# Kernel tuning notes

Hardware: AMD Instinct MI355X
Metric: run time of the kernel (lower is better)

## Reference

```python
import jax, jax.numpy as jnp
import numpy as np

ECNUM = 100
CA1NUM = 100
CA3NUM = 100
ACTNUM = 2
TRACKLEN = 100
SIGMA = 5.0
BS = 4096


def setup_inputs() -> dict:
    key = jax.random.key(0)
    ks = jax.random.split(key, 10)
    cue_train = jax.random.randint(ks[0], (BS, TRACKLEN), 0, 3).astype(jnp.int32) - 1  # values in {-1,0,1}
    ec3_last = jax.random.uniform(ks[1], (BS, ECNUM), dtype=jnp.float32)
    ec5_last = jax.random.uniform(ks[2], (BS, ECNUM), dtype=jnp.float32)
    ca1_last = jnp.zeros((BS, CA1NUM), dtype=jnp.float32)
    cueL = (jax.random.uniform(ks[3], (ECNUM,)) < 0.2).astype(jnp.float32)
    cueR = (jax.random.uniform(ks[4], (ECNUM,)) < 0.2).astype(jnp.float32)
    Wec3ca1 = 0.01 * jax.random.uniform(ks[5], (ECNUM, CA1NUM), dtype=jnp.float32)
    Wca3ca1 = 0.01 * jax.random.uniform(ks[6], (CA3NUM, CA1NUM), dtype=jnp.float32)
    Wca1ec5 = 0.01 * jax.random.normal(ks[7], (CA1NUM, ECNUM), dtype=jnp.float32)
    Wca1act = 0.01 * jax.random.uniform(ks[8], (CA1NUM, ACTNUM), dtype=jnp.float32)
    ca1bias = 0.01 * jax.random.uniform(ks[9], (CA1NUM,), dtype=jnp.float32)
    return {
        "bs": BS,
        "cue_train": cue_train,
        "ec3_last": ec3_last,
        "ec5_last": ec5_last,
        "ca1_last": ca1_last,
        "cueL": cueL,
        "cueR": cueR,
        "Wec3ca1": Wec3ca1,
        "Wca3ca1": Wca3ca1,
        "Wca1ec5": Wca1ec5,
        "Wca1act": Wca1act,
        "ca1bias": ca1bias,
    }


def reference(bs, cue_train, ec3_last, ec5_last, ca1_last, cueL, cueR,
              Wec3ca1, Wca3ca1, Wca1ec5, Wca1act, ca1bias):
    # Precompute position-dependent CA3 activity for every timestep: [T, ca3num]
    centers = jnp.linspace(0.0, float(TRACKLEN), CA3NUM)
    xs = jnp.arange(TRACKLEN, dtype=jnp.float32)
    ca3_all = jnp.exp(-(((xs[:, None] - centers[None, :]) / SIGMA) ** 2) / 2.0)
    drive = ca3_all @ Wca3ca1  # [T, ca1num]

    # Sensory input per timestep via conditional gather: [T, bs, ecnum]
    cue_t = cue_train.T[:, :, None]  # [T, bs, 1]
    sensory = jnp.where(cue_t == 1, cueL[None, None, :],
                        jnp.where(cue_t == -1, cueR[None, None, :], 0.0))

    def step(carry, inp):
        ec3, ec5 = carry
        d, s = inp  # d: [ca1num], s: [bs, ecnum]
        ca1 = jax.nn.relu(d[None, :] * (1.0 + jax.nn.sigmoid(ec3 @ Wec3ca1)) - ca1bias)
        ec5 = ec5 + ca1 @ Wca1ec5
        ec5 = 0.69 + 0.3 * jax.nn.sigmoid(4.0 * (ec5 - 0.3))
        ec3 = ec5 * ec3 + s
        return (ec3, ec5), ca1

    (ec3, ec5), ca1his = jax.lax.scan(step, (ec3_last, ec5_last), (drive, sensory))
    ca1 = ca1his[-1]
    actCell = ca1 @ Wca1act
    return actCell, ca1his, ec3, ec5, ca1
```

## Files before the change

### kernel.cpp

```cpp
#include <hip/hip_runtime.h>

#define TLEN 100
#define ECN  100
#define CA1N 100
#define CA3N 100
#define BSZ  4096
#define ACTN 2
#define BT   16
#define SPF  132
#define SPB  136

typedef short bf16x8 __attribute__((ext_vector_type(8)));
typedef float f32x4  __attribute__((ext_vector_type(4)));

__device__ __forceinline__ unsigned short f2bf(float f){
  union { float f; unsigned int u; } c; c.f = f;
  unsigned int u = c.u;
  unsigned int r = (u + 0x7FFFu + ((u >> 16) & 1u)) >> 16;
  return (unsigned short)r;
}
__device__ __forceinline__ float sigm(float x){ return 1.0f / (1.0f + __expf(-x)); }

__global__ void drive_kernel(const float* __restrict__ Wca3ca1, float* __restrict__ drive){
  __shared__ float ca3row[CA3N];
  const int t = blockIdx.x, tid = threadIdx.x;
  if (tid < CA3N){
    float c = (float)tid * (100.0f / 99.0f);
    float d = ((float)t - c) * 0.2f;
    ca3row[tid] = __expf(-0.5f * d * d);
  }
  __syncthreads();
  if (tid < CA1N){
    float acc = 0.f;
    for (int k = 0; k < CA3N; ++k) acc = fmaf(ca3row[k], Wca3ca1[k*CA1N + tid], acc);
    drive[t*CA1N + tid] = acc;
  }
}

__global__ __launch_bounds__(512, 1)
void rnn_kernel(const int*   __restrict__ cue_train,
                const float* __restrict__ ec3_last,
                const float* __restrict__ ec5_last,
                const float* __restrict__ cueL,
                const float* __restrict__ cueR,
                const float* __restrict__ Wec3ca1,
                const float* __restrict__ Wca1ec5,
                const float* __restrict__ Wca1act,
                const float* __restrict__ ca1bias,
                const float* __restrict__ drive,
                float*       __restrict__ out)
{
  __shared__ __align__(16) float ec3f[BT * SPF];
  __shared__ __align__(16) float ec5f[BT * SPF];
  __shared__ __align__(16) float ca1f[BT * SPF];
  __shared__ __align__(16) unsigned short ec3b[BT * SPB];
  __shared__ __align__(16) unsigned short ca1b[BT * SPB];
  __shared__ signed char cueT[TLEN * BT];

  const int tid = threadIdx.x;
  const int b0  = blockIdx.x * BT;

  float* out_act = out;
  float* out_his = out + (size_t)BSZ * ACTN;
  float* out_e3  = out_his + (size_t)TLEN * BSZ * CA1N;
  float* out_e5  = out_e3 + (size_t)BSZ * ECN;
  float* out_c1  = out_e5 + (size_t)BSZ * ECN;

  for (int idx = tid; idx < BT * SPB; idx += 512){ ec3b[idx] = 0; ca1b[idx] = 0; }
  __syncthreads();

  for (int idx = tid; idx < BT * ECN; idx += 512){
    int r = idx / ECN, c = idx - r * ECN;
    float v3 = ec3_last[(size_t)(b0 + r) * ECN + c];
    ec3f[r * SPF + c] = v3;
    ec3b[r * SPB + c] = f2bf(v3);
    ec5f[r * SPF + c] = ec5_last[(size_t)(b0 + r) * ECN + c];
  }
  for (int idx = tid; idx < BT * TLEN; idx += 512){
    int t = idx >> 4, r = idx & 15;
    cueT[idx] = (signed char)cue_train[(size_t)(b0 + r) * TLEN + t];
  }

  const int lane  = tid & 63;
  const int wv    = tid >> 6;
  const int col16 = lane & 15;
  const int q     = lane >> 4;
  const int col   = wv * 16 + col16;
  const bool okc  = (col < CA1N);

  bf16x8 b1[4], b2[4];
  #pragma unroll
  for (int ks = 0; ks < 4; ++ks){
    #pragma unroll
    for (int jj = 0; jj < 8; ++jj){
      int k = ks * 32 + q * 8 + jj;
      float w1 = 0.f, w2 = 0.f;
      if (k < ECN && okc){
        w1 = Wec3ca1[k * CA1N + col];
        w2 = Wca1ec5[k * ECN  + col];
      }
      b1[ks][jj] = (short)f2bf(w1);
      b2[ks][jj] = (short)f2bf(w2);
    }
  }
  float bias_c = 0.f, cL = 0.f, cR = 0.f;
  if (okc){ bias_c = ca1bias[col]; cL = cueL[col]; cR = cueR[col]; }
  __syncthreads();

  const int m = col16;
  const unsigned short* arow1 = &ec3b[m * SPB];
  const unsigned short* arow2 = &ca1b[m * SPB];

  for (int t = 0; t < TLEN; ++t){
    float dv = okc ? drive[t * CA1N + col] : 0.f;

    f32x4 accA = {0.f,0.f,0.f,0.f}, accB = {0.f,0.f,0.f,0.f};
    {
      bf16x8 a0 = *reinterpret_cast<const bf16x8*>(arow1 +  0 + q * 8);
      bf16x8 a1 = *reinterpret_cast<const bf16x8*>(arow1 + 32 + q * 8);
      bf16x8 a2 = *reinterpret_cast<const bf16x8*>(arow1 + 64 + q * 8);
      bf16x8 a3 = *reinterpret_cast<const bf16x8*>(arow1 + 96 + q * 8);
      accA = __builtin_amdgcn_mfma_f32_16x16x32_bf16(a0, b1[0], accA, 0, 0, 0);
      accB = __builtin_amdgcn_mfma_f32_16x16x32_bf16(a1, b1[1], accB, 0, 0, 0);
      accA = __builtin_amdgcn_mfma_f32_16x16x32_bf16(a2, b1[2], accA, 0, 0, 0);
      accB = __builtin_amdgcn_mfma_f32_16x16x32_bf16(a3, b1[3], accB, 0, 0, 0);
    }
    f32x4 z = accA + accB;
    #pragma unroll
    for (int i = 0; i < 4; ++i){
      int r = q * 4 + i;
      float c1 = fmaxf(fmaf(dv, 1.0f + sigm(z[i]), -bias_c), 0.f);
      if (okc){
        out_his[(size_t)t * (BSZ * CA1N) + (size_t)(b0 + r) * CA1N + col] = c1;
        ca1b[r * SPB + col] = f2bf(c1);
        if (t == TLEN - 1) ca1f[r * SPF + col] = c1;
      }
    }
    __syncthreads();

    f32x4 acc2A = {0.f,0.f,0.f,0.f}, acc2B = {0.f,0.f,0.f,0.f};
    {
      bf16x8 a0 = *reinterpret_cast<const bf16x8*>(arow2 +  0 + q * 8);
      bf16x8 a1 = *reinterpret_cast<const bf16x8*>(arow2 + 32 + q * 8);
      bf16x8 a2 = *reinterpret_cast<const bf16x8*>(arow2 + 64 + q * 8);
      bf16x8 a3 = *reinterpret_cast<const bf16x8*>(arow2 + 96 + q * 8);
      acc2A = __builtin_amdgcn_mfma_f32_16x16x32_bf16(a0, b2[0], acc2A, 0, 0, 0);
      acc2B = __builtin_amdgcn_mfma_f32_16x16x32_bf16(a1, b2[1], acc2B, 0, 0, 0);
      acc2A = __builtin_amdgcn_mfma_f32_16x16x32_bf16(a2, b2[2], acc2A, 0, 0, 0);
      acc2B = __builtin_amdgcn_mfma_f32_16x16x32_bf16(a3, b2[3], acc2B, 0, 0, 0);
    }
    f32x4 z2 = acc2A + acc2B;
    int cu4 = *reinterpret_cast<const int*>(&cueT[t * BT + q * 4]);
    #pragma unroll
    for (int i = 0; i < 4; ++i){
      int r = q * 4 + i;
      if (okc){
        float x  = ec5f[r * SPF + col] + z2[i];
        float e5 = fmaf(0.3f, sigm(fmaf(4.0f, x, -1.2f)), 0.69f);
        ec5f[r * SPF + col] = e5;
        int cu = (int)(signed char)(cu4 >> (8 * i));
        float sns = (cu == 1) ? cL : ((cu == -1) ? cR : 0.0f);
        float e3 = fmaf(e5, ec3f[r * SPF + col], sns);
        ec3f[r * SPF + col] = e3;
        ec3b[r * SPB + col] = f2bf(e3);
      }
    }
    __syncthreads();
  }

  if (tid < BT * ACTN){
    int r = tid >> 1, a = tid & 1;
    float acc = 0.f;
    for (int jj = 0; jj < CA1N; ++jj)
      acc = fmaf(ca1f[r * SPF + jj], Wca1act[jj * ACTN + a], acc);
    out_act[(size_t)(b0 + r) * ACTN + a] = acc;
  }
  for (int idx = tid; idx < BT * ECN; idx += 512){
    int r = idx / ECN, c = idx - r * ECN;
    size_t g = (size_t)(b0 + r) * ECN + c;
    out_e3[g] = ec3f[r * SPF + c];
    out_e5[g] = ec5f[r * SPF + c];
    out_c1[g] = ca1f[r * SPF + c];
  }
}

extern "C" void kernel_launch(void* const* d_in, const int* in_sizes, int n_in,
                              void* d_out, int out_size, void* d_ws, size_t ws_size,
                              hipStream_t stream) {
  (void)in_sizes; (void)n_in; (void)out_size; (void)ws_size;
  const int*   cue_train = (const int*)  d_in[1];
  const float* ec3_last  = (const float*)d_in[2];
  const float* ec5_last  = (const float*)d_in[3];
  const float* cueL      = (const float*)d_in[5];
  const float* cueR      = (const float*)d_in[6];
  const float* Wec3ca1   = (const float*)d_in[7];
  const float* Wca3ca1   = (const float*)d_in[8];
  const float* Wca1ec5   = (const float*)d_in[9];
  const float* Wca1act   = (const float*)d_in[10];
  const float* ca1bias   = (const float*)d_in[11];
  float* out   = (float*)d_out;
  float* drive = (float*)d_ws;

  drive_kernel<<<TLEN, 128, 0, stream>>>(Wca3ca1, drive);
  rnn_kernel<<<BSZ / BT, 512, 0, stream>>>(cue_train, ec3_last, ec5_last,
                                           cueL, cueR, Wec3ca1, Wca1ec5,
                                           Wca1act, ca1bias, drive, out);
}
```

Before: 289.8 us.

## Keep recurrent state in registers and store bf16 operands in MFMA fragment layout

Moves the fp32 ec3/ec5 state from shared memory into per-thread registers. The bf16 operand buffers are stored pre-swizzled in MFMA A-fragment order, so each lane reads one contiguous 16-byte vector. The history store is moved after the barrier, and the idle eighth wave skips the MFMA work. It also simplifies bf16 rounding and the sigmoid (rcp, with the 1+ folded into an fma), and raises launch bounds to allow two blocks per CU. This trims LDS traffic and ALU work on the serial per-step critical path, at the cost of slightly different rounding.

```diff
diff --git a/kernel.cpp b/kernel.cpp
--- a/kernel.cpp
+++ b/kernel.cpp
@@ -7,19 +7,18 @@
 #define BSZ  4096
 #define ACTN 2
 #define BT   16
-#define SPF  132
-#define SPB  136
 
 typedef short bf16x8 __attribute__((ext_vector_type(8)));
 typedef float f32x4  __attribute__((ext_vector_type(4)));
 
 __device__ __forceinline__ unsigned short f2bf(float f){
   union { float f; unsigned int u; } c; c.f = f;
-  unsigned int u = c.u;
-  unsigned int r = (u + 0x7FFFu + ((u >> 16) & 1u)) >> 16;
-  return (unsigned short)r;
-}
-__device__ __forceinline__ float sigm(float x){ return 1.0f / (1.0f + __expf(-x)); }
+  return (unsigned short)((c.u + 0x8000u) >> 16);
+}
+__device__ __forceinline__ float fsigm(float x){
+  float e = __expf(-x);
+  return __builtin_amdgcn_rcpf(1.0f + e);
+}
 
 __global__ void drive_kernel(const float* __restrict__ Wca3ca1, float* __restrict__ drive){
   __shared__ float ca3row[CA3N];
@@ -37,7 +36,8 @@
   }
 }
 
-__global__ __launch_bounds__(512, 1)
+
+__global__ __launch_bounds__(512, 2)
 void rnn_kernel(const int*   __restrict__ cue_train,
                 const float* __restrict__ ec3_last,
                 const float* __restrict__ ec5_last,
@@ -50,11 +50,9 @@
                 const float* __restrict__ drive,
                 float*       __restrict__ out)
 {
-  __shared__ __align__(16) float ec3f[BT * SPF];
-  __shared__ __align__(16) float ec5f[BT * SPF];
-  __shared__ __align__(16) float ca1f[BT * SPF];
-  __shared__ __align__(16) unsigned short ec3b[BT * SPB];
-  __shared__ __align__(16) unsigned short ca1b[BT * SPB];
+  __shared__ __align__(16) unsigned short ec3b[4 * 64 * 8];
+  __shared__ __align__(16) unsigned short ca1b[4 * 64 * 8];
+  __shared__ __align__(16) float ca1f[BT * 132];
   __shared__ signed char cueT[TLEN * BT];
 
   const int tid = threadIdx.x;
@@ -66,16 +64,7 @@
   float* out_e5  = out_e3 + (size_t)BSZ * ECN;
   float* out_c1  = out_e5 + (size_t)BSZ * ECN;
 
-  for (int idx = tid; idx < BT * SPB; idx += 512){ ec3b[idx] = 0; ca1b[idx] = 0; }
-  __syncthreads();
-
-  for (int idx = tid; idx < BT * ECN; idx += 512){
-    int r = idx / ECN, c = idx - r * ECN;
-    float v3 = ec3_last[(size_t)(b0 + r) * ECN + c];
-    ec3f[r * SPF + c] = v3;
-    ec3b[r * SPB + c] = f2bf(v3);
-    ec5f[r * SPF + c] = ec5_last[(size_t)(b0 + r) * ECN + c];
-  }
+  for (int idx = tid; idx < 4 * 64 * 8; idx += 512){ ec3b[idx] = 0; ca1b[idx] = 0; }
   for (int idx = tid; idx < BT * TLEN; idx += 512){
     int t = idx >> 4, r = idx & 15;
     cueT[idx] = (signed char)cue_train[(size_t)(b0 + r) * TLEN + t];
@@ -87,6 +76,10 @@
   const int q     = lane >> 4;
   const int col   = wv * 16 + col16;
   const bool okc  = (col < CA1N);
+  const bool wactive = (wv < 7);
+  const int colc  = okc ? col : 0;
+
+  const int abase = (col >> 5) * 512 + ((col >> 3) & 3) * 128 + (col & 7) + q * 32;
 
   bf16x8 b1[4], b2[4];
   #pragma unroll
@@ -103,84 +96,107 @@
       b2[ks][jj] = (short)f2bf(w2);
     }
   }
-  float bias_c = 0.f, cL = 0.f, cR = 0.f;
-  if (okc){ bias_c = ca1bias[col]; cL = cueL[col]; cR = cueR[col]; }
-  __syncthreads();
-
-  const int m = col16;
-  const unsigned short* arow1 = &ec3b[m * SPB];
-  const unsigned short* arow2 = &ca1b[m * SPB];
+  const float bias_c = okc ? ca1bias[col] : 0.f;
+  const float cL = okc ? cueL[col] : 0.f;
+  const float cR = okc ? cueR[col] : 0.f;
+
+  __syncthreads();
+
+  float ec3v[4], ec5v[4], c1[4] = {0.f,0.f,0.f,0.f};
+  #pragma unroll
+  for (int i = 0; i < 4; ++i){
+    int r = q * 4 + i;
+    float v3 = okc ? ec3_last[(size_t)(b0 + r) * ECN + col] : 0.f;
+    float v5 = okc ? ec5_last[(size_t)(b0 + r) * ECN + col] : 0.f;
+    ec3v[i] = v3; ec5v[i] = v5;
+    if (okc) ec3b[abase + i * 8] = f2bf(v3);
+  }
+  __syncthreads();
+
+  const float* dp = drive + colc;
+  float* hp = out_his + (size_t)(b0 + q * 4) * CA1N + colc;
+
+  const bf16x8* fe3 = (const bf16x8*)ec3b;
+  const bf16x8* fc1 = (const bf16x8*)ca1b;
 
   for (int t = 0; t < TLEN; ++t){
-    float dv = okc ? drive[t * CA1N + col] : 0.f;
-
-    f32x4 accA = {0.f,0.f,0.f,0.f}, accB = {0.f,0.f,0.f,0.f};
-    {
-      bf16x8 a0 = *reinterpret_cast<const bf16x8*>(arow1 +  0 + q * 8);
-      bf16x8 a1 = *reinterpret_cast<const bf16x8*>(arow1 + 32 + q * 8);
-      bf16x8 a2 = *reinterpret_cast<const bf16x8*>(arow1 + 64 + q * 8);
-      bf16x8 a3 = *reinterpret_cast<const bf16x8*>(arow1 + 96 + q * 8);
-      accA = __builtin_amdgcn_mfma_f32_16x16x32_bf16(a0, b1[0], accA, 0, 0, 0);
-      accB = __builtin_amdgcn_mfma_f32_16x16x32_bf16(a1, b1[1], accB, 0, 0, 0);
-      accA = __builtin_amdgcn_mfma_f32_16x16x32_bf16(a2, b1[2], accA, 0, 0, 0);
-      accB = __builtin_amdgcn_mfma_f32_16x16x32_bf16(a3, b1[3], accB, 0, 0, 0);
-    }
-    f32x4 z = accA + accB;
+    float dv  = *dp; dp += CA1N;
+    int   cu4 = *(const int*)(cueT + t * BT + q * 4);
+
+    if (wactive){
+      f32x4 aA = {0.f,0.f,0.f,0.f}, aB = {0.f,0.f,0.f,0.f};
+      bf16x8 a0 = fe3[  0 + lane];
+      bf16x8 a1 = fe3[ 64 + lane];
+      bf16x8 a2 = fe3[128 + lane];
+      bf16x8 a3 = fe3[192 + lane];
+      aA = __builtin_amdgcn_mfma_f32_16x16x32_bf16(a0, b1[0], aA, 0, 0, 0);
+      aB = __builtin_amdgcn_mfma_f32_16x16x32_bf16(a1, b1[1], aB, 0, 0, 0);
+      aA = __builtin_amdgcn_mfma_f32_16x16x32_bf16(a2, b1[2], aA, 0, 0, 0);
+      aB = __builtin_amdgcn_mfma_f32_16x16x32_bf16(a3, b1[3], aB, 0, 0, 0);
+      f32x4 z = aA + aB;
+      float dmb = dv - bias_c;
+      #pragma unroll
+      for (int i = 0; i < 4; ++i){
+        float v = fmaxf(fmaf(dv, fsigm(z[i]), dmb), 0.f);
+        c1[i] = v;
+        if (okc) ca1b[abase + i * 8] = f2bf(v);
+      }
+    }
+    __syncthreads();
+
+    if (okc){
+      hp[0 * CA1N] = c1[0];
+      hp[1 * CA1N] = c1[1];
+      hp[2 * CA1N] = c1[2];
+      hp[3 * CA1N] = c1[3];
+    }
+    hp += (size_t)BSZ * CA1N;
+
+    if (wactive){
+      f32x4 aA = {0.f,0.f,0.f,0.f}, aB = {0.f,0.f,0.f,0.f};
+      bf16x8 a0 = fc1[  0 + lane];
+      bf16x8 a1 = fc1[ 64 + lane];
+      bf16x8 a2 = fc1[128 + lane];
+      bf16x8 a3 = fc1[192 + lane];
+      aA = __builtin_amdgcn_mfma_f32_16x16x32_bf16(a0, b2[0], aA, 0, 0, 0);
+      aB = __builtin_amdgcn_mfma_f32_16x16x32_bf16(a1, b2[1], aB, 0, 0, 0);
+      aA = __builtin_amdgcn_mfma_f32_16x16x32_bf16(a2, b2[2], aA, 0, 0, 0);
+      aB = __builtin_amdgcn_mfma_f32_16x16x32_bf16(a3, b2[3], aB, 0, 0, 0);
+      f32x4 z2 = aA + aB;
+      #pragma unroll
+      for (int i = 0; i < 4; ++i){
+        float x  = ec5v[i] + z2[i];
+        float e5 = fmaf(0.3f, fsigm(fmaf(4.0f, x, -1.2f)), 0.69f);
+        ec5v[i] = e5;
+        int cu = (cu4 >> (8 * i)) & 0xff;
+        float sns = (cu == 1) ? cL : ((cu == 0xff) ? cR : 0.0f);
+        float e3 = fmaf(e5, ec3v[i], sns);
+        ec3v[i] = e3;
+        if (okc) ec3b[abase + i * 8] = f2bf(e3);
+      }
+    }
+    __syncthreads();
+  }
+
+  if (okc){
     #pragma unroll
     for (int i = 0; i < 4; ++i){
       int r = q * 4 + i;
-      float c1 = fmaxf(fmaf(dv, 1.0f + sigm(z[i]), -bias_c), 0.f);
-      if (okc){
-        out_his[(size_t)t * (BSZ * CA1N) + (size_t)(b0 + r) * CA1N + col] = c1;
-        ca1b[r * SPB + col] = f2bf(c1);
-        if (t == TLEN - 1) ca1f[r * SPF + col] = c1;
-      }
-    }
-    __syncthreads();
-
-    f32x4 acc2A = {0.f,0.f,0.f,0.f}, acc2B = {0.f,0.f,0.f,0.f};
-    {
-      bf16x8 a0 = *reinterpret_cast<const bf16x8*>(arow2 +  0 + q * 8);
-      bf16x8 a1 = *reinterpret_cast<const bf16x8*>(arow2 + 32 + q * 8);
-      bf16x8 a2 = *reinterpret_cast<const bf16x8*>(arow2 + 64 + q * 8);
-      bf16x8 a3 = *reinterpret_cast<const bf16x8*>(arow2 + 96 + q * 8);
-      acc2A = __builtin_amdgcn_mfma_f32_16x16x32_bf16(a0, b2[0], acc2A, 0, 0, 0);
-      acc2B = __builtin_amdgcn_mfma_f32_16x16x32_bf16(a1, b2[1], acc2B, 0, 0, 0);
-      acc2A = __builtin_amdgcn_mfma_f32_16x16x32_bf16(a2, b2[2], acc2A, 0, 0, 0);
-      acc2B = __builtin_amdgcn_mfma_f32_16x16x32_bf16(a3, b2[3], acc2B, 0, 0, 0);
-    }
-    f32x4 z2 = acc2A + acc2B;
-    int cu4 = *reinterpret_cast<const int*>(&cueT[t * BT + q * 4]);
-    #pragma unroll
-    for (int i = 0; i < 4; ++i){
-      int r = q * 4 + i;
-      if (okc){
-        float x  = ec5f[r * SPF + col] + z2[i];
-        float e5 = fmaf(0.3f, sigm(fmaf(4.0f, x, -1.2f)), 0.69f);
-        ec5f[r * SPF + col] = e5;
-        int cu = (int)(signed char)(cu4 >> (8 * i));
-        float sns = (cu == 1) ? cL : ((cu == -1) ? cR : 0.0f);
-        float e3 = fmaf(e5, ec3f[r * SPF + col], sns);
-        ec3f[r * SPF + col] = e3;
-        ec3b[r * SPB + col] = f2bf(e3);
-      }
-    }
-    __syncthreads();
-  }
+      size_t g = (size_t)(b0 + r) * ECN + col;
+      out_e3[g] = ec3v[i];
+      out_e5[g] = ec5v[i];
+      out_c1[g] = c1[i];
+      ca1f[r * 132 + col] = c1[i];
+    }
+  }
+  __syncthreads();
 
   if (tid < BT * ACTN){
     int r = tid >> 1, a = tid & 1;
     float acc = 0.f;
     for (int jj = 0; jj < CA1N; ++jj)
-      acc = fmaf(ca1f[r * SPF + jj], Wca1act[jj * ACTN + a], acc);
+      acc = fmaf(ca1f[r * 132 + jj], Wca1act[jj * ACTN + a], acc);
     out_act[(size_t)(b0 + r) * ACTN + a] = acc;
-  }
-  for (int idx = tid; idx < BT * ECN; idx += 512){
-    int r = idx / ECN, c = idx - r * ECN;
-    size_t g = (size_t)(b0 + r) * ECN + c;
-    out_e3[g] = ec3f[r * SPF + c];
-    out_e5[g] = ec5f[r * SPF + c];
-    out_c1[g] = ca1f[r * SPF + c];
   }
 }
 
```

Result: no change. 289.3 us (-0.2%).
